# Optimization experiments

Measured on AMD Instinct MI355X. Metric: run time of the kernel, lower is better.

Reference implementation:

```python
import jax, jax.numpy as jnp
import numpy as np

NEG_SLOPE = 0.2  # keras 'leaky_relu' default negative slope

def _leaky_relu(t):
    return jnp.where(t >= 0, t, NEG_SLOPE * t)

def setup_inputs() -> dict:
    key = jax.random.key(0)
    kx, kq, kk, kv, ko, kg = jax.random.split(key, 6)
    B, H, W, C, A = 4, 64, 64, 256, 128
    x = jax.random.normal(kx, (B, H, W, C), dtype=jnp.float32)
    # 1x1 conv kernels == [Cin, Cout] matrices; glorot-normal-ish scaling
    Wq = jax.random.normal(kq, (C, A), dtype=jnp.float32) * (2.0 / (C + A)) ** 0.5
    Wk = jax.random.normal(kk, (C, A), dtype=jnp.float32) * (2.0 / (C + A)) ** 0.5
    Wv = jax.random.normal(kv, (C, A), dtype=jnp.float32) * (2.0 / (C + A)) ** 0.5
    Wo = jax.random.normal(ko, (A, C), dtype=jnp.float32) * (2.0 / (A + C)) ** 0.5
    # ChannelLearnableMultiplier weight: truncated_normal(0, 0.01) ~ small values near 0
    w_gamma = jax.random.normal(kg, (1, 1, 1, C), dtype=jnp.float32) * 0.01
    return {"x": x, "Wq": Wq, "Wk": Wk, "Wv": Wv, "Wo": Wo, "w_gamma": w_gamma}

def reference(x, Wq, Wk, Wv, Wo, w_gamma):
    B, H, W, C = x.shape
    A = Wq.shape[1]
    # 1x1 conv projections with leaky_relu activation, flatten spatial -> [B, N, A]
    q = _leaky_relu(jnp.einsum('bhwc,ca->bhwa', x, Wq)).reshape(B, H * W, A)
    k = _leaky_relu(jnp.einsum('bhwc,ca->bhwa', x, Wk)).reshape(B, H * W, A)
    v = _leaky_relu(jnp.einsum('bhwc,ca->bhwa', x, Wv)).reshape(B, H * W, A)
    # keras Attention(use_scale=False, score_mode='dot'): softmax(q k^T) v
    scores = jnp.einsum('bnd,bmd->bnm', q, k)          # [B, N, N]
    attn = jax.nn.softmax(scores, axis=-1)
    o = jnp.einsum('bnm,bmd->bnd', attn, v)            # [B, N, A]
    o = o.reshape(B, H, W, A)
    # output 1x1 conv, linear activation
    y = jnp.einsum('bhwa,ac->bhwc', o, Wo)
    # ChannelLearnableMultiplier: tanh(relu(1 + w)) * y
    return jnp.tanh(jax.nn.relu(1.0 + w_gamma)) * y
```

## Files before the change

### kernel.cpp

```cpp
#include <hip/hip_runtime.h>
#include <hip/hip_bf16.h>
#include <cstdint>
#include <cstddef>

typedef __bf16 bf16x8 __attribute__((ext_vector_type(8)));
typedef _Float16 f16x8 __attribute__((ext_vector_type(8)));
typedef short short8 __attribute__((ext_vector_type(8)));
typedef short short4v __attribute__((ext_vector_type(4)));
typedef float f32x4 __attribute__((ext_vector_type(4)));

__device__ __forceinline__ unsigned short f2bf(float f) {
    union { float f; uint32_t u; } v; v.f = f;
    uint32_t u = v.u;
    return (unsigned short)((u + 0x7FFFu + ((u >> 16) & 1u)) >> 16);
}
__device__ __forceinline__ float bf2f(unsigned short h) {
    union { uint32_t u; float f; } v; v.u = ((uint32_t)h) << 16;
    return v.f;
}
__device__ __forceinline__ unsigned short f2h(float f) {
    union { _Float16 h; unsigned short u; } v; v.h = (_Float16)f;
    return v.u;
}

__global__ __launch_bounds__(256) void prep_kernel(
    const float* __restrict__ Wq, const float* __restrict__ Wk,
    const float* __restrict__ Wv, const float* __restrict__ Wo,
    const float* __restrict__ wg,
    unsigned short* __restrict__ wt_hi,
    unsigned short* __restrict__ wt_lo,
    unsigned short* __restrict__ wot,
    float* __restrict__ gamma)
{
    const int bid = blockIdx.x, t = threadIdx.x;
    __shared__ __align__(16) unsigned short Th[128][72], Tl[128][72];
    if (bid < 12) {
        const int proj = bid >> 2, kc = bid & 3;
        const float* W = (proj == 0) ? Wq : ((proj == 1) ? Wk : Wv);
        for (int r = 0; r < 32; ++r) {
            int idx = r * 256 + t;
            int kk = idx >> 7, n = idx & 127;
            float w = W[(size_t)(kc * 64 + kk) * 128 + n];
            unsigned short h = f2bf(w);
            Th[n][kk] = h;
            Tl[n][kk] = f2bf(w - bf2f(h));
        }
        __syncthreads();
        int n = t >> 1, k0 = (t & 1) * 32;
        size_t off = (size_t)proj * 32768 + (size_t)kc * 8192 + (size_t)n * 64 + k0;
        #pragma unroll
        for (int j = 0; j < 4; ++j) {
            *(short8*)(wt_hi + off + j * 8) = *(const short8*)(&Th[n][k0 + j * 8]);
            *(short8*)(wt_lo + off + j * 8) = *(const short8*)(&Tl[n][k0 + j * 8]);
        }
    } else if (bid < 16) {
        const int c0 = (bid - 12) * 64;
        unsigned short* T = &Th[0][0];
        for (int r = 0; r < 32; ++r) {
            int idx = r * 256 + t;
            int a = idx >> 6, cc = idx & 63;
            T[cc * 136 + a] = f2bf(Wo[(size_t)a * 256 + c0 + cc]);
        }
        __syncthreads();
        int cc = t >> 2, a0 = (t & 3) * 32;
        #pragma unroll
        for (int j = 0; j < 4; ++j)
            *(short8*)(wot + (size_t)(c0 + cc) * 128 + a0 + j * 8) =
                *(const short8*)(&T[cc * 136 + a0 + j * 8]);
    } else {
        float g = 1.0f + wg[t];
        if (g < 0.f) g = 0.f;
        gamma[t] = tanhf(g);
    }
}

__global__ __launch_bounds__(256) void qkv_kernel(
    const float* __restrict__ x,
    const unsigned short* __restrict__ wt_hi,
    const unsigned short* __restrict__ wt_lo,
    unsigned short* __restrict__ qkv_ws)
{
    const int rowtile = blockIdx.x;
    const int proj    = blockIdx.y;
    unsigned short* outqk = qkv_ws + (size_t)proj * 2097152u;
    unsigned short* vt    = qkv_ws + (size_t)2 * 2097152u;
    const bool need_lo = (proj < 2);

    const int tid  = threadIdx.x;
    const int lane = tid & 63, wave = tid >> 6;
    const int lo   = lane & 15, quad = lane >> 4;

    __shared__ __align__(16) unsigned short Xh[64][72], Xl[64][72];
    __shared__ __align__(16) unsigned short Wh[128][72], Wl[128][72];

    f32x4 acc[8];
    #pragma unroll
    for (int i = 0; i < 8; ++i) acc[i] = (f32x4){0.f, 0.f, 0.f, 0.f};

    const int wn = tid >> 1, wk0 = (tid & 1) * 32;

    for (int kc = 0; kc < 4; ++kc) {
        __syncthreads();
        #pragma unroll
        for (int i = 0; i < 4; ++i) {
            int flat4 = (i * 256 + tid) * 4;
            int row = flat4 >> 6, col = flat4 & 63;
            float4 tv4 = *(const float4*)(x + (size_t)(rowtile * 64 + row) * 256 + kc * 64 + col);
            float tv[4] = {tv4.x, tv4.y, tv4.z, tv4.w};
            short4v h, l;
            #pragma unroll
            for (int j = 0; j < 4; ++j) {
                unsigned short hj = f2bf(tv[j]);
                h[j] = (short)hj;
                l[j] = (short)f2bf(tv[j] - bf2f(hj));
            }
            *(short4v*)(&Xh[row][col]) = h;
            if (need_lo) *(short4v*)(&Xl[row][col]) = l;
        }
        {
            const size_t off = (size_t)proj * 32768 + (size_t)kc * 8192 + (size_t)wn * 64 + wk0;
            #pragma unroll
            for (int j = 0; j < 4; ++j)
                *(short8*)(&Wh[wn][wk0 + j * 8]) = *(const short8*)(wt_hi + off + j * 8);
            if (need_lo) {
                #pragma unroll
                for (int j = 0; j < 4; ++j)
                    *(short8*)(&Wl[wn][wk0 + j * 8]) = *(const short8*)(wt_lo + off + j * 8);
            }
        }
        __syncthreads();
        #pragma unroll
        for (int ks = 0; ks < 2; ++ks) {
            bf16x8 ah = *(const bf16x8*)(&Xh[wave * 16 + lo][ks * 32 + quad * 8]);
            #pragma unroll
            for (int nb = 0; nb < 8; ++nb) {
                bf16x8 bh = *(const bf16x8*)(&Wh[nb * 16 + lo][ks * 32 + quad * 8]);
                acc[nb] = __builtin_amdgcn_mfma_f32_16x16x32_bf16(ah, bh, acc[nb], 0, 0, 0);
                if (need_lo) {
                    bf16x8 al = *(const bf16x8*)(&Xl[wave * 16 + lo][ks * 32 + quad * 8]);
                    bf16x8 bl = *(const bf16x8*)(&Wl[nb * 16 + lo][ks * 32 + quad * 8]);
                    acc[nb] = __builtin_amdgcn_mfma_f32_16x16x32_bf16(al, bh, acc[nb], 0, 0, 0);
                    acc[nb] = __builtin_amdgcn_mfma_f32_16x16x32_bf16(ah, bl, acc[nb], 0, 0, 0);
                }
            }
        }
    }
    if (proj < 2) {
        #pragma unroll
        for (int nb = 0; nb < 8; ++nb) {
            #pragma unroll
            for (int r = 0; r < 4; ++r) {
                float v = acc[nb][r];
                v = (v >= 0.f) ? v : 0.2f * v;
                int m = rowtile * 64 + wave * 16 + quad * 4 + r;
                outqk[(size_t)m * 128 + nb * 16 + lo] = f2h(v);
            }
        }
    } else {
        const int b  = rowtile >> 6;
        const int sb = (rowtile & 63) * 64;
        #pragma unroll
        for (int nb = 0; nb < 8; ++nb) {
            #pragma unroll
            for (int r = 0; r < 4; ++r) {
                float v = acc[nb][r];
                v = (v >= 0.f) ? v : 0.2f * v;
                int seq = sb + wave * 16 + quad * 4 + r;
                int d   = nb * 16 + lo;
                vt[(size_t)b * 524288 + (size_t)d * 4096 + seq] = f2bf(v);
            }
        }
    }
}

__global__ __launch_bounds__(256) void attn_kernel(
    const unsigned short* __restrict__ qkv_ws,
    unsigned short* __restrict__ part,
    float* __restrict__ lpart,
    int chunk)
{
    const int b  = blockIdx.x;
    const int qt = blockIdx.y;
    const int z  = blockIdx.z;
    const int tid  = threadIdx.x;
    const int lane = tid & 63, wave = tid >> 6;
    const int lo   = lane & 15, quad = lane >> 4;

    const unsigned short* q  = qkv_ws;
    const unsigned short* k  = qkv_ws + 2097152u;
    const unsigned short* vt = qkv_ws + (size_t)2 * 2097152u + (size_t)b * 524288u;

    __shared__ __align__(16) unsigned short Ks[2][32][136];
    __shared__ __align__(16) unsigned short Vt4[2][4][128][8];
    __shared__ __align__(16) unsigned short Ps[4][32][40];

    const int qbase = qt * 128 + wave * 32;
    f16x8 qf[2][4];
    #pragma unroll
    for (int g = 0; g < 2; ++g)
        #pragma unroll
        for (int ks = 0; ks < 4; ++ks)
            qf[g][ks] = *(const f16x8*)(q + ((size_t)(b * 4096 + qbase + g * 16 + lo)) * 128
                                          + ks * 32 + quad * 8);

    f32x4 oacc[2][8];
    #pragma unroll
    for (int g = 0; g < 2; ++g)
        #pragma unroll
        for (int i = 0; i < 8; ++i) oacc[g][i] = (f32x4){0.f, 0.f, 0.f, 0.f};
    float lsum[2][4];
    #pragma unroll
    for (int g = 0; g < 2; ++g)
        #pragma unroll
        for (int r = 0; r < 4; ++r) lsum[g][r] = 1e-30f;

    const float LOG2E  = 1.44269504088896f;
    const float NSHIFT = -40.0f * 1.44269504088896f;

    const int krow0 = tid >> 4, kcol0 = (tid & 15) * 8;
    const int krow1 = 16 + (tid >> 4);
    const int vd = tid >> 2, vc = tid & 3;

    const int niter = chunk >> 5;
    const int sbase = z * chunk;

    short8 ka, kb, va, vb;
    ka = *(const short8*)(k + ((size_t)(b * 4096 + sbase + krow0)) * 128 + kcol0);
    kb = *(const short8*)(k + ((size_t)(b * 4096 + sbase + krow1)) * 128 + kcol0);
    va = *(const short8*)(vt + (size_t)vd * 4096 + sbase + vc * 8);
    vb = *(const short8*)(vt + (size_t)(vd + 64) * 4096 + sbase + vc * 8);
    *(short8*)(&Ks[0][krow0][kcol0]) = ka;
    *(short8*)(&Ks[0][krow1][kcol0]) = kb;
    *(short8*)(&Vt4[0][vc][vd][0]) = va;
    *(short8*)(&Vt4[0][vc][vd + 64][0]) = vb;
    __syncthreads();

    for (int kt = 0; kt < niter; ++kt) {
        const int cur = kt & 1, nxt = cur ^ 1;
        const bool more = (kt + 1 < niter);
        if (more) {
            const int s1 = sbase + (kt + 1) * 32;
            ka = *(const short8*)(k + ((size_t)(b * 4096 + s1 + krow0)) * 128 + kcol0);
            kb = *(const short8*)(k + ((size_t)(b * 4096 + s1 + krow1)) * 128 + kcol0);
            va = *(const short8*)(vt + (size_t)vd * 4096 + s1 + vc * 8);
            vb = *(const short8*)(vt + (size_t)(vd + 64) * 4096 + s1 + vc * 8);
        }

        f32x4 s[2][2];
        s[0][0] = (f32x4){0.f,0.f,0.f,0.f}; s[0][1] = (f32x4){0.f,0.f,0.f,0.f};
        s[1][0] = (f32x4){0.f,0.f,0.f,0.f}; s[1][1] = (f32x4){0.f,0.f,0.f,0.f};
        #pragma unroll
        for (int ks = 0; ks < 4; ++ks) {
            #pragma unroll
            for (int nb = 0; nb < 2; ++nb) {
                f16x8 bf = *(const f16x8*)(&Ks[cur][nb * 16 + lo][ks * 32 + quad * 8]);
                s[0][nb] = __builtin_amdgcn_mfma_f32_16x16x32_f16(qf[0][ks], bf, s[0][nb], 0, 0, 0);
                s[1][nb] = __builtin_amdgcn_mfma_f32_16x16x32_f16(qf[1][ks], bf, s[1][nb], 0, 0, 0);
            }
        }
        #pragma unroll
        for (int g = 0; g < 2; ++g) {
            #pragma unroll
            for (int nb = 0; nb < 2; ++nb) {
                #pragma unroll
                for (int r = 0; r < 4; ++r) {
                    float t = fminf(fmaf(s[g][nb][r], LOG2E, NSHIFT), 125.0f);
                    union { float f; uint32_t u; } pv; pv.f = exp2f(t);
                    unsigned short pt = (unsigned short)(pv.u >> 16);
                    lsum[g][r] += bf2f(pt);
                    Ps[wave][g * 16 + quad * 4 + r][nb * 16 + lo] = pt;
                }
            }
        }
        bf16x8 pf0 = *(const bf16x8*)(&Ps[wave][lo][quad * 8]);
        bf16x8 pf1 = *(const bf16x8*)(&Ps[wave][16 + lo][quad * 8]);
        #pragma unroll
        for (int nb = 0; nb < 8; ++nb) {
            bf16x8 vf = *(const bf16x8*)(&Vt4[cur][quad][nb * 16 + lo][0]);
            oacc[0][nb] = __builtin_amdgcn_mfma_f32_16x16x32_bf16(pf0, vf, oacc[0][nb], 0, 0, 0);
            oacc[1][nb] = __builtin_amdgcn_mfma_f32_16x16x32_bf16(pf1, vf, oacc[1][nb], 0, 0, 0);
        }
        if (more) {
            *(short8*)(&Ks[nxt][krow0][kcol0]) = ka;
            *(short8*)(&Ks[nxt][krow1][kcol0]) = kb;
            *(short8*)(&Vt4[nxt][vc][vd][0]) = va;
            *(short8*)(&Vt4[nxt][vc][vd + 64][0]) = vb;
        }
        __syncthreads();
    }

    #pragma unroll
    for (int g = 0; g < 2; ++g) {
        #pragma unroll
        for (int r = 0; r < 4; ++r) {
            float xr = lsum[g][r];
            #pragma unroll
            for (int m = 1; m < 16; m <<= 1) xr += __shfl_xor(xr, m, 64);
            lsum[g][r] = xr;
        }
        #pragma unroll
        for (int nb = 0; nb < 8; ++nb) {
            #pragma unroll
            for (int r = 0; r < 4; ++r) {
                int m = b * 4096 + qbase + g * 16 + quad * 4 + r;
                part[((size_t)z * 16384 + m) * 128 + nb * 16 + lo] = f2bf(oacc[g][nb][r]);
            }
        }
        if (lo == 0) {
            #pragma unroll
            for (int r = 0; r < 4; ++r) {
                int m = b * 4096 + qbase + g * 16 + quad * 4 + r;
                lpart[(size_t)z * 16384 + m] = lsum[g][r];
            }
        }
    }
}

__global__ __launch_bounds__(256) void outproj_kernel(
    const unsigned short* __restrict__ part,
    const float* __restrict__ lpart,
    const unsigned short* __restrict__ wot,
    const float* __restrict__ gamma,
    float* __restrict__ out,
    int nsplit)
{
    const int rowtile = blockIdx.x;
    const int tid  = threadIdx.x;
    const int lane = tid & 63, wave = tid >> 6;
    const int lo   = lane & 15, quad = lane >> 4;

    __shared__ __align__(16) unsigned short Os[64][136];
    __shared__ __align__(16) unsigned short WoT[128][136];

    #pragma unroll
    for (int i = 0; i < 4; ++i) {
        int flat = (i * 256 + tid) * 8;
        int row = flat >> 7, col = flat & 127;
        int m = rowtile * 64 + row;
        float acc8[8] = {0.f,0.f,0.f,0.f,0.f,0.f,0.f,0.f};
        float l = 0.f;
        for (int zz = 0; zz < nsplit; ++zz) {
            short8 t = *(const short8*)(part + ((size_t)zz * 16384 + m) * 128 + col);
            #pragma unroll
            for (int j = 0; j < 8; ++j) acc8[j] += bf2f((unsigned short)t[j]);
            l += lpart[(size_t)zz * 16384 + m];
        }
        float inv = 1.0f / l;
        short8 o8;
        #pragma unroll
        for (int j = 0; j < 8; ++j) o8[j] = (short)f2bf(acc8[j] * inv);
        *(short8*)(&Os[row][col]) = o8;
    }

    const int wc = tid >> 1, wa0 = (tid & 1) * 64;
    for (int ch = 0; ch < 2; ++ch) {
        if (ch) __syncthreads();
        #pragma unroll
        for (int j = 0; j < 8; ++j)
            *(short8*)(&WoT[wc][wa0 + j * 8]) =
                *(const short8*)(wot + (size_t)(ch * 128 + wc) * 128 + wa0 + j * 8);
        __syncthreads();

        f32x4 acc[8];
        #pragma unroll
        for (int i = 0; i < 8; ++i) acc[i] = (f32x4){0.f, 0.f, 0.f, 0.f};
        #pragma unroll
        for (int ks = 0; ks < 4; ++ks) {
            bf16x8 a = *(const bf16x8*)(&Os[wave * 16 + lo][ks * 32 + quad * 8]);
            #pragma unroll
            for (int nb = 0; nb < 8; ++nb) {
                bf16x8 bf = *(const bf16x8*)(&WoT[nb * 16 + lo][ks * 32 + quad * 8]);
                acc[nb] = __builtin_amdgcn_mfma_f32_16x16x32_bf16(a, bf, acc[nb], 0, 0, 0);
            }
        }
        #pragma unroll
        for (int nb = 0; nb < 8; ++nb) {
            int c = ch * 128 + nb * 16 + lo;
            float g = gamma[c];
            #pragma unroll
            for (int r = 0; r < 4; ++r) {
                int m = rowtile * 64 + wave * 16 + quad * 4 + r;
                out[(size_t)m * 256 + c] = acc[nb][r] * g;
            }
        }
    }
}

extern "C" void kernel_launch(void* const* d_in, const int* in_sizes, int n_in,
                              void* d_out, int out_size, void* d_ws, size_t ws_size,
                              hipStream_t stream) {
    const float* x  = (const float*)d_in[0];
    const float* Wq = (const float*)d_in[1];
    const float* Wk = (const float*)d_in[2];
    const float* Wv = (const float*)d_in[3];
    const float* Wo = (const float*)d_in[4];
    const float* wg = (const float*)d_in[5];
    float* out = (float*)d_out;

    unsigned short* ws = (unsigned short*)d_ws;
    const int nsplit = (ws_size >= (size_t)47000000) ? 8 : 4;
    const int chunk  = 4096 / nsplit;

    unsigned short* qkv_ws = ws;
    unsigned short* part   = ws + (size_t)3 * 2097152u;
    unsigned short* wt_hi  = part;
    unsigned short* wt_lo  = part + 98304u;
    float* lpart = (float*)(part + (size_t)nsplit * 2097152u);
    unsigned short* wot = (unsigned short*)(lpart + (size_t)nsplit * 16384u);
    float* gamma = (float*)(wot + 32768u);

    prep_kernel<<<dim3(17), 256, 0, stream>>>(Wq, Wk, Wv, Wo, wg, wt_hi, wt_lo, wot, gamma);
    qkv_kernel<<<dim3(256, 3), 256, 0, stream>>>(x, wt_hi, wt_lo, qkv_ws);
    attn_kernel<<<dim3(4, 32, nsplit), 256, 0, stream>>>(qkv_ws, part, lpart, chunk);
    outproj_kernel<<<dim3(256), 256, 0, stream>>>(part, lpart, wot, gamma, out, nsplit);
}
```

Baseline: 181.3 us.

## Compute transposed scores to keep P in registers, removing LDS round-trip

```diff
diff --git a/kernel.cpp b/kernel.cpp
--- a/kernel.cpp
+++ b/kernel.cpp
@@ -8,6 +8,16 @@
 typedef short short8 __attribute__((ext_vector_type(8)));
 typedef short short4v __attribute__((ext_vector_type(4)));
 typedef float f32x4 __attribute__((ext_vector_type(4)));
+
+#if __has_builtin(__builtin_amdgcn_mfma_f32_16x16x16bf16_1k)
+  #define HAVE_K16 1
+  #define MFMA16BF(a,b,c) __builtin_amdgcn_mfma_f32_16x16x16bf16_1k((a),(b),(c),0,0,0)
+#elif __has_builtin(__builtin_amdgcn_mfma_f32_16x16x16_bf16)
+  #define HAVE_K16 1
+  #define MFMA16BF(a,b,c) __builtin_amdgcn_mfma_f32_16x16x16_bf16((a),(b),(c),0,0,0)
+#else
+  #define HAVE_K16 0
+#endif
 
 __device__ __forceinline__ unsigned short f2bf(float f) {
     union { float f; uint32_t u; } v; v.f = f;
@@ -173,6 +183,7 @@
     }
 }
 
+#if HAVE_K16
 __global__ __launch_bounds__(256) void attn_kernel(
     const unsigned short* __restrict__ qkv_ws,
     unsigned short* __restrict__ part,
@@ -190,9 +201,8 @@
     const unsigned short* k  = qkv_ws + 2097152u;
     const unsigned short* vt = qkv_ws + (size_t)2 * 2097152u + (size_t)b * 524288u;
 
-    __shared__ __align__(16) unsigned short Ks[2][32][136];
-    __shared__ __align__(16) unsigned short Vt4[2][4][128][8];
-    __shared__ __align__(16) unsigned short Ps[4][32][40];
+    __shared__ __align__(16) unsigned short Ks[32][136];
+    __shared__ __align__(16) unsigned short Vt[128][40];
 
     const int qbase = qt * 128 + wave * 32;
     f16x8 qf[2][4];
@@ -208,11 +218,7 @@
     for (int g = 0; g < 2; ++g)
         #pragma unroll
         for (int i = 0; i < 8; ++i) oacc[g][i] = (f32x4){0.f, 0.f, 0.f, 0.f};
-    float lsum[2][4];
-    #pragma unroll
-    for (int g = 0; g < 2; ++g)
-        #pragma unroll
-        for (int r = 0; r < 4; ++r) lsum[g][r] = 1e-30f;
+    float Lsum[2] = {1e-30f, 1e-30f};
 
     const float LOG2E  = 1.44269504088896f;
     const float NSHIFT = -40.0f * 1.44269504088896f;
@@ -220,6 +226,9 @@
     const int krow0 = tid >> 4, kcol0 = (tid & 15) * 8;
     const int krow1 = 16 + (tid >> 4);
     const int vd = tid >> 2, vc = tid & 3;
+    const int vst  = vc >> 1;
+    const int colA = ((2 * vc) & 3) * 8 + vst * 4;
+    const int colB = ((2 * vc + 1) & 3) * 8 + vst * 4;
 
     const int niter = chunk >> 5;
     const int sbase = z * chunk;
@@ -229,16 +238,21 @@
     kb = *(const short8*)(k + ((size_t)(b * 4096 + sbase + krow1)) * 128 + kcol0);
     va = *(const short8*)(vt + (size_t)vd * 4096 + sbase + vc * 8);
     vb = *(const short8*)(vt + (size_t)(vd + 64) * 4096 + sbase + vc * 8);
-    *(short8*)(&Ks[0][krow0][kcol0]) = ka;
-    *(short8*)(&Ks[0][krow1][kcol0]) = kb;
-    *(short8*)(&Vt4[0][vc][vd][0]) = va;
-    *(short8*)(&Vt4[0][vc][vd + 64][0]) = vb;
-    __syncthreads();
 
     for (int kt = 0; kt < niter; ++kt) {
-        const int cur = kt & 1, nxt = cur ^ 1;
-        const bool more = (kt + 1 < niter);
-        if (more) {
+        __syncthreads();
+        *(short8*)(&Ks[krow0][kcol0]) = ka;
+        *(short8*)(&Ks[krow1][kcol0]) = kb;
+        {
+            short4v a0 = {va[0], va[1], va[2], va[3]}, a1 = {va[4], va[5], va[6], va[7]};
+            short4v b0 = {vb[0], vb[1], vb[2], vb[3]}, b1 = {vb[4], vb[5], vb[6], vb[7]};
+            *(short4v*)(&Vt[vd][colA])      = a0;
+            *(short4v*)(&Vt[vd][colB])      = a1;
+            *(short4v*)(&Vt[vd + 64][colA]) = b0;
+            *(short4v*)(&Vt[vd + 64][colB]) = b1;
+        }
+        __syncthreads();
+        if (kt + 1 < niter) {
             const int s1 = sbase + (kt + 1) * 32;
             ka = *(const short8*)(k + ((size_t)(b * 4096 + s1 + krow0)) * 128 + kcol0);
             kb = *(const short8*)(k + ((size_t)(b * 4096 + s1 + krow1)) * 128 + kcol0);
@@ -246,6 +260,140 @@
             vb = *(const short8*)(vt + (size_t)(vd + 64) * 4096 + s1 + vc * 8);
         }
 
+        f32x4 sT[2][2];
+        sT[0][0] = (f32x4){0.f,0.f,0.f,0.f}; sT[0][1] = (f32x4){0.f,0.f,0.f,0.f};
+        sT[1][0] = (f32x4){0.f,0.f,0.f,0.f}; sT[1][1] = (f32x4){0.f,0.f,0.f,0.f};
+        #pragma unroll
+        for (int ks = 0; ks < 4; ++ks) {
+            #pragma unroll
+            for (int st = 0; st < 2; ++st) {
+                f16x8 kf = *(const f16x8*)(&Ks[st * 16 + lo][ks * 32 + quad * 8]);
+                sT[0][st] = __builtin_amdgcn_mfma_f32_16x16x32_f16(kf, qf[0][ks], sT[0][st], 0, 0, 0);
+                sT[1][st] = __builtin_amdgcn_mfma_f32_16x16x32_f16(kf, qf[1][ks], sT[1][st], 0, 0, 0);
+            }
+        }
+        short4v Pp[2][2];
+        #pragma unroll
+        for (int g = 0; g < 2; ++g) {
+            #pragma unroll
+            for (int st = 0; st < 2; ++st) {
+                #pragma unroll
+                for (int r = 0; r < 4; ++r) {
+                    float t = fminf(fmaf(sT[g][st][r], LOG2E, NSHIFT), 125.0f);
+                    union { float f; uint32_t u; } pv; pv.f = exp2f(t);
+                    unsigned short pt = (unsigned short)(pv.u >> 16);
+                    Lsum[g] += bf2f(pt);
+                    Pp[g][st][r] = (short)pt;
+                }
+            }
+        }
+        #pragma unroll
+        for (int nb = 0; nb < 8; ++nb) {
+            short8 vv = *(const short8*)(&Vt[nb * 16 + lo][quad * 8]);
+            short4v v0 = {vv[0], vv[1], vv[2], vv[3]};
+            short4v v1 = {vv[4], vv[5], vv[6], vv[7]};
+            #pragma unroll
+            for (int g = 0; g < 2; ++g) {
+                oacc[g][nb] = MFMA16BF(Pp[g][0], v0, oacc[g][nb]);
+                oacc[g][nb] = MFMA16BF(Pp[g][1], v1, oacc[g][nb]);
+            }
+        }
+    }
+
+    #pragma unroll
+    for (int g = 0; g < 2; ++g) {
+        float xr = Lsum[g];
+        xr += __shfl_xor(xr, 16, 64);
+        xr += __shfl_xor(xr, 32, 64);
+        Lsum[g] = xr;
+    }
+    #pragma unroll
+    for (int g = 0; g < 2; ++g) {
+        #pragma unroll
+        for (int nb = 0; nb < 8; ++nb) {
+            #pragma unroll
+            for (int r = 0; r < 4; ++r) {
+                int m = b * 4096 + qbase + g * 16 + quad * 4 + r;
+                part[((size_t)z * 16384 + m) * 128 + nb * 16 + lo] = f2bf(oacc[g][nb][r]);
+            }
+        }
+        if (lane < 16) {
+            int m = b * 4096 + qbase + g * 16 + lane;
+            lpart[(size_t)z * 16384 + m] = Lsum[g];
+        }
+    }
+}
+#else
+__global__ __launch_bounds__(256) void attn_kernel(
+    const unsigned short* __restrict__ qkv_ws,
+    unsigned short* __restrict__ part,
+    float* __restrict__ lpart,
+    int chunk)
+{
+    const int b  = blockIdx.x;
+    const int qt = blockIdx.y;
+    const int z  = blockIdx.z;
+    const int tid  = threadIdx.x;
+    const int lane = tid & 63, wave = tid >> 6;
+    const int lo   = lane & 15, quad = lane >> 4;
+
+    const unsigned short* q  = qkv_ws;
+    const unsigned short* k  = qkv_ws + 2097152u;
+    const unsigned short* vt = qkv_ws + (size_t)2 * 2097152u + (size_t)b * 524288u;
+
+    __shared__ __align__(16) unsigned short Ks[32][136];
+    __shared__ __align__(16) unsigned short Vt[128][40];
+    __shared__ __align__(16) unsigned short Ps[4][32][40];
+
+    const int qbase = qt * 128 + wave * 32;
+    f16x8 qf[2][4];
+    #pragma unroll
+    for (int g = 0; g < 2; ++g)
+        #pragma unroll
+        for (int ks = 0; ks < 4; ++ks)
+            qf[g][ks] = *(const f16x8*)(q + ((size_t)(b * 4096 + qbase + g * 16 + lo)) * 128
+                                          + ks * 32 + quad * 8);
+    f32x4 oacc[2][8];
+    #pragma unroll
+    for (int g = 0; g < 2; ++g)
+        #pragma unroll
+        for (int i = 0; i < 8; ++i) oacc[g][i] = (f32x4){0.f, 0.f, 0.f, 0.f};
+    float lsum[2][4];
+    #pragma unroll
+    for (int g = 0; g < 2; ++g)
+        #pragma unroll
+        for (int r = 0; r < 4; ++r) lsum[g][r] = 1e-30f;
+
+    const float LOG2E  = 1.44269504088896f;
+    const float NSHIFT = -40.0f * 1.44269504088896f;
+
+    const int krow0 = tid >> 4, kcol0 = (tid & 15) * 8;
+    const int krow1 = 16 + (tid >> 4);
+    const int vd0 = tid >> 2, vs0 = (tid & 3) * 8;
+
+    const int niter = chunk >> 5;
+    const int sbase = z * chunk;
+
+    short8 ka, kb, va, vb;
+    ka = *(const short8*)(k + ((size_t)(b * 4096 + sbase + krow0)) * 128 + kcol0);
+    kb = *(const short8*)(k + ((size_t)(b * 4096 + sbase + krow1)) * 128 + kcol0);
+    va = *(const short8*)(vt + (size_t)vd0 * 4096 + sbase + vs0);
+    vb = *(const short8*)(vt + (size_t)(vd0 + 64) * 4096 + sbase + vs0);
+
+    for (int kt = 0; kt < niter; ++kt) {
+        __syncthreads();
+        *(short8*)(&Ks[krow0][kcol0]) = ka;
+        *(short8*)(&Ks[krow1][kcol0]) = kb;
+        *(short8*)(&Vt[vd0][vs0]) = va;
+        *(short8*)(&Vt[vd0 + 64][vs0]) = vb;
+        __syncthreads();
+        if (kt + 1 < niter) {
+            const int s1 = sbase + (kt + 1) * 32;
+            ka = *(const short8*)(k + ((size_t)(b * 4096 + s1 + krow0)) * 128 + kcol0);
+            kb = *(const short8*)(k + ((size_t)(b * 4096 + s1 + krow1)) * 128 + kcol0);
+            va = *(const short8*)(vt + (size_t)vd0 * 4096 + s1 + vs0);
+            vb = *(const short8*)(vt + (size_t)(vd0 + 64) * 4096 + s1 + vs0);
+        }
         f32x4 s[2][2];
         s[0][0] = (f32x4){0.f,0.f,0.f,0.f}; s[0][1] = (f32x4){0.f,0.f,0.f,0.f};
         s[1][0] = (f32x4){0.f,0.f,0.f,0.f}; s[1][1] = (f32x4){0.f,0.f,0.f,0.f};
@@ -253,15 +401,15 @@
         for (int ks = 0; ks < 4; ++ks) {
             #pragma unroll
             for (int nb = 0; nb < 2; ++nb) {
-                f16x8 bf = *(const f16x8*)(&Ks[cur][nb * 16 + lo][ks * 32 + quad * 8]);
+                f16x8 bf = *(const f16x8*)(&Ks[nb * 16 + lo][ks * 32 + quad * 8]);
                 s[0][nb] = __builtin_amdgcn_mfma_f32_16x16x32_f16(qf[0][ks], bf, s[0][nb], 0, 0, 0);
                 s[1][nb] = __builtin_amdgcn_mfma_f32_16x16x32_f16(qf[1][ks], bf, s[1][nb], 0, 0, 0);
             }
         }
         #pragma unroll
-        for (int g = 0; g < 2; ++g) {
-            #pragma unroll
-            for (int nb = 0; nb < 2; ++nb) {
+        for (int g = 0; g < 2; ++g)
+            #pragma unroll
+            for (int nb = 0; nb < 2; ++nb)
                 #pragma unroll
                 for (int r = 0; r < 4; ++r) {
                     float t = fminf(fmaf(s[g][nb][r], LOG2E, NSHIFT), 125.0f);
@@ -270,25 +418,15 @@
                     lsum[g][r] += bf2f(pt);
                     Ps[wave][g * 16 + quad * 4 + r][nb * 16 + lo] = pt;
                 }
-            }
-        }
         bf16x8 pf0 = *(const bf16x8*)(&Ps[wave][lo][quad * 8]);
         bf16x8 pf1 = *(const bf16x8*)(&Ps[wave][16 + lo][quad * 8]);
         #pragma unroll
         for (int nb = 0; nb < 8; ++nb) {
-            bf16x8 vf = *(const bf16x8*)(&Vt4[cur][quad][nb * 16 + lo][0]);
+            bf16x8 vf = *(const bf16x8*)(&Vt[nb * 16 + lo][quad * 8]);
             oacc[0][nb] = __builtin_amdgcn_mfma_f32_16x16x32_bf16(pf0, vf, oacc[0][nb], 0, 0, 0);
             oacc[1][nb] = __builtin_amdgcn_mfma_f32_16x16x32_bf16(pf1, vf, oacc[1][nb], 0, 0, 0);
         }
-        if (more) {
-            *(short8*)(&Ks[nxt][krow0][kcol0]) = ka;
-            *(short8*)(&Ks[nxt][krow1][kcol0]) = kb;
-            *(short8*)(&Vt4[nxt][vc][vd][0]) = va;
-            *(short8*)(&Vt4[nxt][vc][vd + 64][0]) = vb;
-        }
-        __syncthreads();
-    }
-
+    }
     #pragma unroll
     for (int g = 0; g < 2; ++g) {
         #pragma unroll
@@ -299,22 +437,21 @@
             lsum[g][r] = xr;
         }
         #pragma unroll
-        for (int nb = 0; nb < 8; ++nb) {
+        for (int nb = 0; nb < 8; ++nb)
             #pragma unroll
             for (int r = 0; r < 4; ++r) {
                 int m = b * 4096 + qbase + g * 16 + quad * 4 + r;
                 part[((size_t)z * 16384 + m) * 128 + nb * 16 + lo] = f2bf(oacc[g][nb][r]);
             }
-        }
-        if (lo == 0) {
+        if (lo == 0)
             #pragma unroll
             for (int r = 0; r < 4; ++r) {
                 int m = b * 4096 + qbase + g * 16 + quad * 4 + r;
                 lpart[(size_t)z * 16384 + m] = lsum[g][r];
             }
-        }
-    }
-}
+    }
+}
+#endif
 
 __global__ __launch_bounds__(256) void outproj_kernel(
     const unsigned short* __restrict__ part,
```

After: 178.1 us. No clear change (-1.8%).

## Compute transposed scores to keep P in registers and drop LDS staging

Applied to the files above, without the earlier changes.

```diff
diff --git a/kernel.cpp b/kernel.cpp
--- a/kernel.cpp
+++ b/kernel.cpp
@@ -8,6 +8,22 @@
 typedef short short8 __attribute__((ext_vector_type(8)));
 typedef short short4v __attribute__((ext_vector_type(4)));
 typedef float f32x4 __attribute__((ext_vector_type(4)));
+
+#if defined(__HIP_DEVICE_COMPILE__)
+  #define MFMA16BF(a,b,c) __builtin_amdgcn_mfma_f32_16x16x16bf16_1k((a),(b),(c),0,0,0)
+  #define MFMA32F16(a,b,c) __builtin_amdgcn_mfma_f32_16x16x32_f16((a),(b),(c),0,0,0)
+  #define MFMA32BF(a,b,c)  __builtin_amdgcn_mfma_f32_16x16x32_bf16((a),(b),(c),0,0,0)
+#else
+  #define MFMA16BF(a,b,c)  (c)
+  #define MFMA32F16(a,b,c) (c)
+  #define MFMA32BF(a,b,c)  (c)
+#endif
+
+#if defined(__HIP_DEVICE_COMPILE__) && __has_builtin(__builtin_amdgcn_exp2f)
+  #define EXP2F(x) __builtin_amdgcn_exp2f(x)
+#else
+  #define EXP2F(x) exp2f(x)
+#endif
 
 __device__ __forceinline__ unsigned short f2bf(float f) {
     union { float f; uint32_t u; } v; v.f = f;
@@ -83,7 +99,7 @@
     const int rowtile = blockIdx.x;
     const int proj    = blockIdx.y;
     unsigned short* outqk = qkv_ws + (size_t)proj * 2097152u;
-    unsigned short* vt    = qkv_ws + (size_t)2 * 2097152u;
+    unsigned short* vp    = qkv_ws + (size_t)2 * 2097152u;
     const bool need_lo = (proj < 2);
 
     const int tid  = threadIdx.x;
@@ -135,12 +151,12 @@
             #pragma unroll
             for (int nb = 0; nb < 8; ++nb) {
                 bf16x8 bh = *(const bf16x8*)(&Wh[nb * 16 + lo][ks * 32 + quad * 8]);
-                acc[nb] = __builtin_amdgcn_mfma_f32_16x16x32_bf16(ah, bh, acc[nb], 0, 0, 0);
+                acc[nb] = MFMA32BF(ah, bh, acc[nb]);
                 if (need_lo) {
                     bf16x8 al = *(const bf16x8*)(&Xl[wave * 16 + lo][ks * 32 + quad * 8]);
                     bf16x8 bl = *(const bf16x8*)(&Wl[nb * 16 + lo][ks * 32 + quad * 8]);
-                    acc[nb] = __builtin_amdgcn_mfma_f32_16x16x32_bf16(al, bh, acc[nb], 0, 0, 0);
-                    acc[nb] = __builtin_amdgcn_mfma_f32_16x16x32_bf16(ah, bl, acc[nb], 0, 0, 0);
+                    acc[nb] = MFMA32BF(al, bh, acc[nb]);
+                    acc[nb] = MFMA32BF(ah, bl, acc[nb]);
                 }
             }
         }
@@ -158,17 +174,18 @@
         }
     } else {
         const int b  = rowtile >> 6;
-        const int sb = (rowtile & 63) * 64;
+        const int sc = ((rowtile & 63) << 4) + wave * 4 + quad;
+        unsigned short* vpb = vp + (size_t)b * 524288u + (size_t)sc * 512u;
         #pragma unroll
         for (int nb = 0; nb < 8; ++nb) {
+            short4v o4;
             #pragma unroll
             for (int r = 0; r < 4; ++r) {
                 float v = acc[nb][r];
                 v = (v >= 0.f) ? v : 0.2f * v;
-                int seq = sb + wave * 16 + quad * 4 + r;
-                int d   = nb * 16 + lo;
-                vt[(size_t)b * 524288 + (size_t)d * 4096 + seq] = f2bf(v);
-            }
+                o4[r] = (short)f2bf(v);
+            }
+            *(short4v*)(vpb + (size_t)(nb * 16 + lo) * 4) = o4;
         }
     }
 }
@@ -188,11 +205,7 @@
 
     const unsigned short* q  = qkv_ws;
     const unsigned short* k  = qkv_ws + 2097152u;
-    const unsigned short* vt = qkv_ws + (size_t)2 * 2097152u + (size_t)b * 524288u;
-
-    __shared__ __align__(16) unsigned short Ks[2][32][136];
-    __shared__ __align__(16) unsigned short Vt4[2][4][128][8];
-    __shared__ __align__(16) unsigned short Ps[4][32][40];
+    const unsigned short* vp = qkv_ws + (size_t)2 * 2097152u + (size_t)b * 524288u;
 
     const int qbase = qt * 128 + wave * 32;
     f16x8 qf[2][4];
@@ -208,96 +221,75 @@
     for (int g = 0; g < 2; ++g)
         #pragma unroll
         for (int i = 0; i < 8; ++i) oacc[g][i] = (f32x4){0.f, 0.f, 0.f, 0.f};
-    float lsum[2][4];
-    #pragma unroll
-    for (int g = 0; g < 2; ++g)
-        #pragma unroll
-        for (int r = 0; r < 4; ++r) lsum[g][r] = 1e-30f;
+    float Lsum[2] = {1e-30f, 1e-30f};
 
     const float LOG2E  = 1.44269504088896f;
     const float NSHIFT = -40.0f * 1.44269504088896f;
 
-    const int krow0 = tid >> 4, kcol0 = (tid & 15) * 8;
-    const int krow1 = 16 + (tid >> 4);
-    const int vd = tid >> 2, vc = tid & 3;
-
     const int niter = chunk >> 5;
     const int sbase = z * chunk;
 
-    short8 ka, kb, va, vb;
-    ka = *(const short8*)(k + ((size_t)(b * 4096 + sbase + krow0)) * 128 + kcol0);
-    kb = *(const short8*)(k + ((size_t)(b * 4096 + sbase + krow1)) * 128 + kcol0);
-    va = *(const short8*)(vt + (size_t)vd * 4096 + sbase + vc * 8);
-    vb = *(const short8*)(vt + (size_t)(vd + 64) * 4096 + sbase + vc * 8);
-    *(short8*)(&Ks[0][krow0][kcol0]) = ka;
-    *(short8*)(&Ks[0][krow1][kcol0]) = kb;
-    *(short8*)(&Vt4[0][vc][vd][0]) = va;
-    *(short8*)(&Vt4[0][vc][vd + 64][0]) = vb;
-    __syncthreads();
+    const unsigned short* kbase = k + ((size_t)(b * 4096 + sbase + lo)) * 128 + quad * 8;
 
     for (int kt = 0; kt < niter; ++kt) {
-        const int cur = kt & 1, nxt = cur ^ 1;
-        const bool more = (kt + 1 < niter);
-        if (more) {
-            const int s1 = sbase + (kt + 1) * 32;
-            ka = *(const short8*)(k + ((size_t)(b * 4096 + s1 + krow0)) * 128 + kcol0);
-            kb = *(const short8*)(k + ((size_t)(b * 4096 + s1 + krow1)) * 128 + kcol0);
-            va = *(const short8*)(vt + (size_t)vd * 4096 + s1 + vc * 8);
-            vb = *(const short8*)(vt + (size_t)(vd + 64) * 4096 + s1 + vc * 8);
-        }
-
-        f32x4 s[2][2];
-        s[0][0] = (f32x4){0.f,0.f,0.f,0.f}; s[0][1] = (f32x4){0.f,0.f,0.f,0.f};
-        s[1][0] = (f32x4){0.f,0.f,0.f,0.f}; s[1][1] = (f32x4){0.f,0.f,0.f,0.f};
-        #pragma unroll
-        for (int ks = 0; ks < 4; ++ks) {
-            #pragma unroll
-            for (int nb = 0; nb < 2; ++nb) {
-                f16x8 bf = *(const f16x8*)(&Ks[cur][nb * 16 + lo][ks * 32 + quad * 8]);
-                s[0][nb] = __builtin_amdgcn_mfma_f32_16x16x32_f16(qf[0][ks], bf, s[0][nb], 0, 0, 0);
-                s[1][nb] = __builtin_amdgcn_mfma_f32_16x16x32_f16(qf[1][ks], bf, s[1][nb], 0, 0, 0);
-            }
-        }
+        const int s0 = kt * 32;
+
+        f32x4 sT[2][2];
+        sT[0][0] = (f32x4){0.f,0.f,0.f,0.f}; sT[0][1] = (f32x4){0.f,0.f,0.f,0.f};
+        sT[1][0] = (f32x4){0.f,0.f,0.f,0.f}; sT[1][1] = (f32x4){0.f,0.f,0.f,0.f};
+        #pragma unroll
+        for (int st = 0; st < 2; ++st) {
+            const unsigned short* krow = kbase + (size_t)(s0 + st * 16) * 128;
+            #pragma unroll
+            for (int ks = 0; ks < 4; ++ks) {
+                f16x8 kf = *(const f16x8*)(krow + ks * 32);
+                sT[0][st] = MFMA32F16(kf, qf[0][ks], sT[0][st]);
+                sT[1][st] = MFMA32F16(kf, qf[1][ks], sT[1][st]);
+            }
+        }
+        short4v vf[2][8];
+        #pragma unroll
+        for (int st = 0; st < 2; ++st) {
+            const int sc = ((sbase + s0 + st * 16) >> 2) + quad;
+            const unsigned short* vrow = vp + (size_t)sc * 512u + (size_t)lo * 4;
+            #pragma unroll
+            for (int nb = 0; nb < 8; ++nb)
+                vf[st][nb] = *(const short4v*)(vrow + nb * 64);
+        }
+        short4v Pp[2][2];
         #pragma unroll
         for (int g = 0; g < 2; ++g) {
             #pragma unroll
-            for (int nb = 0; nb < 2; ++nb) {
+            for (int st = 0; st < 2; ++st) {
                 #pragma unroll
                 for (int r = 0; r < 4; ++r) {
-                    float t = fminf(fmaf(s[g][nb][r], LOG2E, NSHIFT), 125.0f);
-                    union { float f; uint32_t u; } pv; pv.f = exp2f(t);
+                    float t = fminf(fmaf(sT[g][st][r], LOG2E, NSHIFT), 125.0f);
+                    union { float f; uint32_t u; } pv; pv.f = EXP2F(t);
                     unsigned short pt = (unsigned short)(pv.u >> 16);
-                    lsum[g][r] += bf2f(pt);
-                    Ps[wave][g * 16 + quad * 4 + r][nb * 16 + lo] = pt;
+                    Lsum[g] += bf2f(pt);
+                    Pp[g][st][r] = (short)pt;
                 }
             }
         }
-        bf16x8 pf0 = *(const bf16x8*)(&Ps[wave][lo][quad * 8]);
-        bf16x8 pf1 = *(const bf16x8*)(&Ps[wave][16 + lo][quad * 8]);
         #pragma unroll
         for (int nb = 0; nb < 8; ++nb) {
-            bf16x8 vf = *(const bf16x8*)(&Vt4[cur][quad][nb * 16 + lo][0]);
-            oacc[0][nb] = __builtin_amdgcn_mfma_f32_16x16x32_bf16(pf0, vf, oacc[0][nb], 0, 0, 0);
-            oacc[1][nb] = __builtin_amdgcn_mfma_f32_16x16x32_bf16(pf1, vf, oacc[1][nb], 0, 0, 0);
-        }
-        if (more) {
-            *(short8*)(&Ks[nxt][krow0][kcol0]) = ka;
-            *(short8*)(&Ks[nxt][krow1][kcol0]) = kb;
-            *(short8*)(&Vt4[nxt][vc][vd][0]) = va;
-            *(short8*)(&Vt4[nxt][vc][vd + 64][0]) = vb;
-        }
-        __syncthreads();
+            #pragma unroll
+            for (int g = 0; g < 2; ++g) {
+                oacc[g][nb] = MFMA16BF(Pp[g][0], vf[0][nb], oacc[g][nb]);
+                oacc[g][nb] = MFMA16BF(Pp[g][1], vf[1][nb], oacc[g][nb]);
+            }
+        }
     }
 
     #pragma unroll
     for (int g = 0; g < 2; ++g) {
-        #pragma unroll
-        for (int r = 0; r < 4; ++r) {
-            float xr = lsum[g][r];
-            #pragma unroll
-            for (int m = 1; m < 16; m <<= 1) xr += __shfl_xor(xr, m, 64);
-            lsum[g][r] = xr;
-        }
+        float xr = Lsum[g];
+        xr += __shfl_xor(xr, 16, 64);
+        xr += __shfl_xor(xr, 32, 64);
+        Lsum[g] = xr;
+    }
+    #pragma unroll
+    for (int g = 0; g < 2; ++g) {
         #pragma unroll
         for (int nb = 0; nb < 8; ++nb) {
             #pragma unroll
@@ -306,12 +298,9 @@
                 part[((size_t)z * 16384 + m) * 128 + nb * 16 + lo] = f2bf(oacc[g][nb][r]);
             }
         }
-        if (lo == 0) {
-            #pragma unroll
-            for (int r = 0; r < 4; ++r) {
-                int m = b * 4096 + qbase + g * 16 + quad * 4 + r;
-                lpart[(size_t)z * 16384 + m] = lsum[g][r];
-            }
+        if (lane < 16) {
+            int m = b * 4096 + qbase + g * 16 + lane;
+            lpart[(size_t)z * 16384 + m] = Lsum[g];
         }
     }
 }
@@ -370,7 +359,7 @@
             #pragma unroll
             for (int nb = 0; nb < 8; ++nb) {
                 bf16x8 bf = *(const bf16x8*)(&WoT[nb * 16 + lo][ks * 32 + quad * 8]);
-                acc[nb] = __builtin_amdgcn_mfma_f32_16x16x32_bf16(a, bf, acc[nb], 0, 0, 0);
+                acc[nb] = MFMA32BF(a, bf, acc[nb]);
             }
         }
         #pragma unroll
```

After: 218.2 us. 20.4% more time.
